# Kernel tuning notes

Measured on AMD Instinct MI355X. Metric: run time of the kernel, lower is better.

## Reference

```python
import jax, jax.numpy as jnp
import numpy as np

NEG_SLOPE = 0.2  # PyG GATConv default
EPS = 1e-16      # PyG softmax denominator epsilon

N_NODES = 100000
N_EDGES = 1600000
NFEAT = 768
NHID = 128
N_GRAPHS = 128


def setup_inputs() -> dict:
    key = jax.random.key(0)
    ks = jax.random.split(key, 12)
    x = jax.random.normal(ks[0], (N_NODES, NFEAT), dtype=jnp.float32)
    edge_index = jax.random.randint(ks[1], (2, N_EDGES), 0, N_NODES, dtype=jnp.int64)
    batch = jnp.sort(jax.random.randint(ks[2], (N_NODES,), 0, N_GRAPHS, dtype=jnp.int64))
    s = 1.0 / np.sqrt(NFEAT)
    sh = 1.0 / np.sqrt(NHID)
    params = {
        'W': jax.random.normal(ks[3], (NFEAT, NHID), dtype=jnp.float32) * s,
        'att_src': jax.random.normal(ks[4], (NHID,), dtype=jnp.float32) * sh,
        'att_dst': jax.random.normal(ks[5], (NHID,), dtype=jnp.float32) * sh,
        'b_conv': jnp.zeros((NHID,), dtype=jnp.float32),
        'W0': jax.random.normal(ks[6], (NFEAT, NHID), dtype=jnp.float32) * s,
        'b0': jnp.zeros((NHID,), dtype=jnp.float32),
        'W1': jax.random.normal(ks[7], (2 * NHID, NHID), dtype=jnp.float32) * sh,
        'b1': jnp.zeros((NHID,), dtype=jnp.float32),
        'W2': jax.random.normal(ks[8], (NHID, 2), dtype=jnp.float32) * sh,
        'b2': jnp.zeros((2,), dtype=jnp.float32),
    }
    return dict(x=x, edge_index=edge_index, batch=batch, num_graphs=N_GRAPHS, **params)


def _gat_conv(x, edge_index, W, att_src, att_dst, b_conv):
    N = x.shape[0]
    h = x @ W                               # [N, nhid]
    # add self loops (PyG default)
    loop = jnp.arange(N, dtype=edge_index.dtype)
    src = jnp.concatenate([edge_index[0], loop])
    dst = jnp.concatenate([edge_index[1], loop])
    a_src = h @ att_src                     # [N]
    a_dst = h @ att_dst                     # [N]
    e = a_src[src] + a_dst[dst]             # [E+N]
    e = jnp.where(e > 0, e, NEG_SLOPE * e)  # leaky relu
    # segment softmax over edges grouped by destination node
    m = jax.ops.segment_max(e, dst, num_segments=N)
    expe = jnp.exp(e - m[dst])
    denom = jax.ops.segment_sum(expe, dst, num_segments=N)
    alpha = expe / (denom[dst] + EPS)       # [E+N]
    out = jax.ops.segment_sum(alpha[:, None] * h[src], dst, num_segments=N)
    return out + b_conv


def reference(x, edge_index, batch, num_graphs, W, att_src, att_dst, b_conv,
              W0, b0, W1, b1, W2, b2):
    h = jax.nn.relu(_gat_conv(x, edge_index, W, att_src, att_dst, b_conv))  # [N, nhid]
    # global max pool per graph
    x1 = jax.ops.segment_max(h, batch, num_segments=num_graphs)             # [G, nhid]
    # root node of each graph = first node with batch == idx (batch sorted)
    roots = jnp.searchsorted(batch, jnp.arange(num_graphs, dtype=batch.dtype))
    news = jax.nn.relu(x[roots] @ W0 + b0)                                  # [G, nhid]
    z = jnp.concatenate([x1, news], axis=1)                                 # [G, 2*nhid]
    z = jax.nn.relu(z @ W1 + b1)
    logp = jax.nn.log_softmax(z @ W2 + b2, axis=1)                          # [G, 2]
    return (logp, x1, logp)
```

## Files before the change

kernel.cpp:

```cpp
#include <hip/hip_runtime.h>
#include <hip/hip_bf16.h>

#define NFEAT 768
#define NHID 128
#define NEG_SLOPE 0.2f
#define SM_EPS 1e-16f
#define CAP 96

#define BROWS 32
#define QSTRIDE 200

#define BSH 7
#define BNODES 128
#define CAPB 3072

#define SMEM_BYTES 26624

typedef __attribute__((ext_vector_type(8))) short bf16x8s;
typedef __attribute__((ext_vector_type(4))) float f32x4;

__device__ inline float bf2f(unsigned short u) {
    return __uint_as_float(((unsigned int)u) << 16);
}
__device__ inline unsigned short f2bf(float f) {
    union { __hip_bfloat16 b; unsigned short u; } c;
    c.b = __float2bfloat16(f);
    return c.u;
}
__device__ inline ushort4 cvt4(float4 v) {
    union { ushort4 u4; __hip_bfloat162 h[2]; } u;
    u.h[0] = __float22bfloat162_rn(float2{v.x, v.y});
    u.h[1] = __float22bfloat162_rn(float2{v.z, v.w});
    return u.u4;
}

__global__ void prep_wt(const float* __restrict__ W, unsigned short* __restrict__ Wt) {
    int idx = blockIdx.x * 256 + threadIdx.x;
    if (idx >= NFEAT * NHID) return;
    int k = idx >> 7, n = idx & 127;
    Wt[(size_t)n * NFEAT + k] = f2bf(W[idx]);
}

__global__ __launch_bounds__(256) void gemm_scatter_k(
        const float* __restrict__ x, const unsigned short* __restrict__ Wt,
        const float* __restrict__ att_src, const float* __restrict__ att_dst,
        unsigned short* __restrict__ hbf, float* __restrict__ a_src,
        float* __restrict__ a_dst, int M, int GB,
        const int* __restrict__ esrc, const int* __restrict__ edst,
        int* __restrict__ bktCnt, int* __restrict__ ebkt, int E, int nbkt) {
    __shared__ __align__(16) unsigned char smem[SMEM_BYTES];
    const int tid = threadIdx.x;

    if (blockIdx.x < GB) {
        unsigned short* At = (unsigned short*)smem;
        float* asum = (float*)(smem + 25600);
        const int lane = tid & 63;
        const int wid = tid >> 6;
        const int r0 = blockIdx.x * BROWS;
        if (r0 >= M) return;

        int qrow[6], qcol[6];
#pragma unroll
        for (int i = 0; i < 6; ++i) {
            int idx = i * 256 + tid;
            qrow[i] = idx / 48;
            qcol[i] = (idx % 48) * 4;
        }
        float4 xbuf[6];
        auto qload = [&](int q) {
#pragma unroll
            for (int i = 0; i < 6; ++i) {
                int gr = r0 + qrow[i]; if (gr >= M) gr = M - 1;
                xbuf[i] = *(const float4*)(x + (size_t)gr * NFEAT + q * 192 + qcol[i]);
            }
        };
        auto qwrite = [&](int q) {
#pragma unroll
            for (int i = 0; i < 6; ++i)
                *(ushort4*)(&At[(q & 1) * (BROWS * QSTRIDE) + qrow[i] * QSTRIDE + qcol[i]]) = cvt4(xbuf[i]);
        };

        const int rl = lane & 15;
        const int kc = (lane >> 4) * 8;
        const int c0 = wid * 32;
        const unsigned short* bp0 = Wt + (size_t)(c0 + rl) * NFEAT + kc;
        const unsigned short* bp1 = bp0 + (size_t)16 * NFEAT;

        qload(0); qwrite(0);
        __syncthreads();

        f32x4 acc[2][2] = {};
#pragma unroll
        for (int q = 0; q < 4; ++q) {
            bf16x8s bq0[6], bq1[6];
#pragma unroll
            for (int l = 0; l < 6; ++l) {
                int ks = q * 6 + l;
                bq0[l] = *(const bf16x8s*)(bp0 + ks * 32);
                bq1[l] = *(const bf16x8s*)(bp1 + ks * 32);
            }
            if (q < 3) qload(q + 1);
            const unsigned short* A0 = &At[(q & 1) * (BROWS * QSTRIDE) + rl * QSTRIDE + kc];
            const unsigned short* A1 = A0 + 16 * QSTRIDE;
#pragma unroll
            for (int l = 0; l < 6; ++l) {
                bf16x8s a0 = *(const bf16x8s*)(A0 + l * 32);
                bf16x8s a1 = *(const bf16x8s*)(A1 + l * 32);
                acc[0][0] = __builtin_amdgcn_mfma_f32_16x16x32_bf16(a0, bq0[l], acc[0][0], 0, 0, 0);
                acc[0][1] = __builtin_amdgcn_mfma_f32_16x16x32_bf16(a0, bq1[l], acc[0][1], 0, 0, 0);
                acc[1][0] = __builtin_amdgcn_mfma_f32_16x16x32_bf16(a1, bq0[l], acc[1][0], 0, 0, 0);
                acc[1][1] = __builtin_amdgcn_mfma_f32_16x16x32_bf16(a1, bq1[l], acc[1][1], 0, 0, 0);
            }
            if (q < 3) { qwrite(q + 1); __syncthreads(); }
        }

        const int cc = lane & 15;
        const int cg = lane >> 4;
        float as_[2], ad_[2];
#pragma unroll
        for (int n = 0; n < 2; ++n) {
            as_[n] = att_src[c0 + n * 16 + cc];
            ad_[n] = att_dst[c0 + n * 16 + cc];
        }
#pragma unroll
        for (int mfr = 0; mfr < 2; ++mfr) {
#pragma unroll
            for (int j = 0; j < 4; ++j) {
                int row = mfr * 16 + cg * 4 + j;
                int gr = r0 + row;
                float ps = 0.f, pd = 0.f;
#pragma unroll
                for (int n = 0; n < 2; ++n) {
                    float v = acc[mfr][n][j];
                    if (gr < M) hbf[(size_t)gr * NHID + c0 + n * 16 + cc] = f2bf(v);
                    ps += v * as_[n]; pd += v * ad_[n];
                }
#pragma unroll
                for (int d = 1; d < 16; d <<= 1) { ps += __shfl_xor(ps, d); pd += __shfl_xor(pd, d); }
                if (cc == 0) { asum[(0 * 4 + wid) * BROWS + row] = ps; asum[(1 * 4 + wid) * BROWS + row] = pd; }
            }
        }
        __syncthreads();
        if (tid < 64) {
            int row = tid & 31, sd = tid >> 5;
            float v = asum[(sd * 4 + 0) * BROWS + row] + asum[(sd * 4 + 1) * BROWS + row]
                    + asum[(sd * 4 + 2) * BROWS + row] + asum[(sd * 4 + 3) * BROWS + row];
            int gr = r0 + row;
            if (gr < M) { if (sd) a_dst[gr] = v; else a_src[gr] = v; }
        }
    } else {
        int* hist = (int*)smem;
        int* base = hist + 1024;
        int* curs = base + 1024;
        const int bid = blockIdx.x - GB;
        const int e0 = bid * 2048 + tid * 8;
        for (int b = tid; b < nbkt; b += 256) hist[b] = 0;
        __syncthreads();

        int dv[8], sv[8];
        int nval = 0;
        if (e0 + 7 < E) {
            int4 d0 = *(const int4*)(edst + e0), d1 = *(const int4*)(edst + e0 + 4);
            int4 s0 = *(const int4*)(esrc + e0), s1 = *(const int4*)(esrc + e0 + 4);
            dv[0] = d0.x; dv[1] = d0.y; dv[2] = d0.z; dv[3] = d0.w;
            dv[4] = d1.x; dv[5] = d1.y; dv[6] = d1.z; dv[7] = d1.w;
            sv[0] = s0.x; sv[1] = s0.y; sv[2] = s0.z; sv[3] = s0.w;
            sv[4] = s1.x; sv[5] = s1.y; sv[6] = s1.z; sv[7] = s1.w;
            nval = 8;
        } else {
            for (int i = 0; i < 8; ++i) {
                int e = e0 + i;
                if (e < E) { dv[nval] = edst[e]; sv[nval] = esrc[e]; ++nval; }
            }
        }
        for (int i = 0; i < nval; ++i) atomicAdd(&hist[dv[i] >> BSH], 1);
        __syncthreads();
        for (int b = tid; b < nbkt; b += 256) {
            int h = hist[b];
            if (h) base[b] = atomicAdd(bktCnt + b, h);
            curs[b] = 0;
        }
        __syncthreads();
        for (int i = 0; i < nval; ++i) {
            int b = dv[i] >> BSH;
            int pos = base[b] + atomicAdd(&curs[b], 1);
            if (pos < CAPB)
                ebkt[(size_t)b * CAPB + pos] = ((dv[i] & (BNODES - 1)) << 18) | sv[i];
        }
    }
}

__global__ __launch_bounds__(128) void csrb_k(const int* __restrict__ bktCnt,
                                              const int* __restrict__ ebkt,
                                              int* __restrict__ deg, int* __restrict__ off,
                                              int* __restrict__ csr, int N) {
    __shared__ int hist[BNODES], scn[BNODES], curs[BNODES];
    const int b = blockIdx.x, t = threadIdx.x;
    const int cnt = min(bktCnt[b], CAPB);
    const int* eb = ebkt + (size_t)b * CAPB;
    const int csrb = b * (CAPB + BNODES);
    const int node = (b << BSH) + t;

    hist[t] = 0;
    __syncthreads();
    for (int i = t; i < cnt; i += BNODES) atomicAdd(&hist[eb[i] >> 18], 1);
    __syncthreads();
    int tot = hist[t] + (node < N ? 1 : 0);
    scn[t] = tot;
    __syncthreads();
    for (int d = 1; d < BNODES; d <<= 1) {
        int x = (t >= d) ? scn[t - d] : 0;
        __syncthreads();
        scn[t] += x;
        __syncthreads();
    }
    int excl = scn[t] - tot;
    if (node < N) { deg[node] = tot; off[node] = csrb + excl; }
    curs[t] = excl;
    __syncthreads();
    for (int i = t; i < cnt; i += BNODES) {
        int v = eb[i];
        int pos = atomicAdd(&curs[v >> 18], 1);
        csr[csrb + pos] = v & 0x3FFFF;
    }
    __syncthreads();
    if (node < N) csr[csrb + curs[t]] = node;
}

__global__ __launch_bounds__(256) void aggregate_k(const int* __restrict__ off,
                                                   const int* __restrict__ deg,
                                                   const int* __restrict__ csr,
                                                   const float* __restrict__ a_src,
                                                   const float* __restrict__ a_dst,
                                                   const unsigned short* __restrict__ hbf,
                                                   const float* __restrict__ b_conv,
                                                   unsigned short* __restrict__ hrelu, int N) {
    __shared__ int   ssh[4][CAP];
    __shared__ float wsh[4][CAP];
    int wid = threadIdx.x >> 6, lane = threadIdx.x & 63;
    int dst = blockIdx.x * 4 + wid;
    if (dst >= N) return;
    int start = off[dst], cnt = deg[dst];
    float ad = a_dst[dst];

    float m = -1e30f;
    for (int j = lane; j < cnt; j += 64) {
        int s = csr[start + j];
        float e = a_src[s] + ad;
        e = e > 0.f ? e : NEG_SLOPE * e;
        if (j < CAP) { ssh[wid][j] = s; wsh[wid][j] = e; }
        m = fmaxf(m, e);
    }
#pragma unroll
    for (int d = 32; d; d >>= 1) m = fmaxf(m, __shfl_xor(m, d));

    float denom = 0.f;
    for (int j = lane; j < cnt; j += 64) {
        float e;
        if (j < CAP) e = wsh[wid][j];
        else {
            int s = csr[start + j];
            e = a_src[s] + ad;
            e = e > 0.f ? e : NEG_SLOPE * e;
        }
        float w = __expf(e - m);
        if (j < CAP) wsh[wid][j] = w;
        denom += w;
    }
#pragma unroll
    for (int d = 32; d; d >>= 1) denom += __shfl_xor(denom, d);

    const int el = lane >> 4;
    const int fg = lane & 15;
    float acc[8] = {};
    const unsigned short* hp8 = hbf + fg * 8;

    auto fma8 = [&](int s, float w) {
        bf16x8s hv = *(const bf16x8s*)(hp8 + (size_t)s * NHID);
#pragma unroll
        for (int i = 0; i < 8; ++i)
            acc[i] += w * bf2f((unsigned short)hv[i]);
    };

    if (cnt <= CAP) {
        int quads = cnt >> 2;
#pragma unroll 2
        for (int p = 0; p < quads; ++p) {
            int jj = p * 4 + el;
            fma8(ssh[wid][jj], wsh[wid][jj]);
        }
        int rem = cnt & 3;
        if (rem) {
            int jb = cnt & ~3;
            int jj = jb + (el < rem ? el : 0);
            float w = (el < rem) ? wsh[wid][jj] : 0.f;
            fma8(ssh[wid][jj], w);
        }
    } else {
        for (int j = 0; j < cnt; j += 4) {
            int jj = j + el;
            int s; float w;
            if (jj < cnt) {
                if (jj < CAP) { s = ssh[wid][jj]; w = wsh[wid][jj]; }
                else {
                    s = csr[start + jj];
                    float e = a_src[s] + ad;
                    e = e > 0.f ? e : NEG_SLOPE * e;
                    w = __expf(e - m);
                }
            } else { s = ssh[wid][0]; w = 0.f; }
            fma8(s, w);
        }
    }
#pragma unroll
    for (int i = 0; i < 8; ++i) {
        acc[i] += __shfl_xor(acc[i], 16);
        acc[i] += __shfl_xor(acc[i], 32);
    }

    if (lane < 16) {
        float inv = 1.f / (denom + SM_EPS);
        union { bf16x8s v; unsigned short u[8]; } ob;
#pragma unroll
        for (int i = 0; i < 8; ++i)
            ob.u[i] = f2bf(fmaxf(acc[i] * inv + b_conv[fg * 8 + i], 0.f));
        *(bf16x8s*)(&hrelu[(size_t)dst * NHID + fg * 8]) = ob.v;
    }
}

__global__ __launch_bounds__(256) void pool_max(const unsigned short* __restrict__ hrelu,
                                                const int* __restrict__ batch,
                                                float* __restrict__ x1, int N) {
    int wid = threadIdx.x >> 6, lane = threadIdx.x & 63;
    int n0 = blockIdx.x * 256 + wid * 64;
    if (n0 >= N) return;
    int gcur = batch[n0];
    float v0 = 0.f, v1 = 0.f;
    int end = min(n0 + 64, N);
    for (int n = n0; n < end; ++n) {
        int g = batch[n];
        if (g != gcur) {
            atomicMax((int*)&x1[gcur * NHID + lane * 2],     __float_as_int(v0));
            atomicMax((int*)&x1[gcur * NHID + lane * 2 + 1], __float_as_int(v1));
            v0 = v1 = 0.f; gcur = g;
        }
        ushort2 hv = *(const ushort2*)(hrelu + (size_t)n * NHID + lane * 2);
        v0 = fmaxf(v0, bf2f(hv.x)); v1 = fmaxf(v1, bf2f(hv.y));
    }
    atomicMax((int*)&x1[gcur * NHID + lane * 2],     __float_as_int(v0));
    atomicMax((int*)&x1[gcur * NHID + lane * 2 + 1], __float_as_int(v1));
}

__global__ __launch_bounds__(128) void tail_k(const float* __restrict__ x,
                                              const int* __restrict__ batch,
                                              const float* __restrict__ W0,
                                              const float* __restrict__ b0,
                                              const float* __restrict__ W1,
                                              const float* __restrict__ b1,
                                              const float* __restrict__ W2,
                                              const float* __restrict__ b2,
                                              const float* __restrict__ x1,
                                              float* __restrict__ logp0,
                                              float* __restrict__ logp1, int N) {
    __shared__ float xr[NFEAT];
    __shared__ float zin[2 * NHID];
    __shared__ float z[NHID];
    __shared__ float lg[2];
    int g = blockIdx.x, t = threadIdx.x;
    int lo = 0, hi = N;
    while (lo < hi) { int mid = (lo + hi) >> 1; if (batch[mid] < g) lo = mid + 1; else hi = mid; }
    int root = min(lo, N - 1);
    const float* xp = x + (size_t)root * NFEAT;
    for (int i = t; i < NFEAT; i += 128) xr[i] = xp[i];
    zin[t] = x1[(size_t)g * NHID + t];
    __syncthreads();
    float acc = b0[t];
#pragma unroll 8
    for (int k = 0; k < NFEAT; ++k) acc += xr[k] * W0[(size_t)k * NHID + t];
    zin[NHID + t] = fmaxf(acc, 0.f);
    __syncthreads();
    float a1 = b1[t];
#pragma unroll 8
    for (int k = 0; k < 2 * NHID; ++k) a1 += zin[k] * W1[(size_t)k * NHID + t];
    z[t] = fmaxf(a1, 0.f);
    __syncthreads();
    if (t < 2) {
        float a = b2[t];
        for (int k = 0; k < NHID; ++k) a += z[k] * W2[k * 2 + t];
        lg[t] = a;
    }
    __syncthreads();
    if (t == 0) {
        float mx = fmaxf(lg[0], lg[1]);
        float lse = mx + logf(expf(lg[0] - mx) + expf(lg[1] - mx));
        float p0 = lg[0] - lse, p1 = lg[1] - lse;
        logp0[g * 2] = p0; logp0[g * 2 + 1] = p1;
        logp1[g * 2] = p0; logp1[g * 2 + 1] = p1;
    }
}

extern "C" void kernel_launch(void* const* d_in, const int* in_sizes, int n_in,
                              void* d_out, int out_size, void* d_ws, size_t ws_size,
                              hipStream_t stream) {
    const float* x        = (const float*)d_in[0];
    const int*   eidx     = (const int*)d_in[1];
    const int*   batch    = (const int*)d_in[2];
    const float* W        = (const float*)d_in[4];
    const float* att_src  = (const float*)d_in[5];
    const float* att_dst  = (const float*)d_in[6];
    const float* b_conv   = (const float*)d_in[7];
    const float* W0       = (const float*)d_in[8];
    const float* b0       = (const float*)d_in[9];
    const float* W1       = (const float*)d_in[10];
    const float* b1       = (const float*)d_in[11];
    const float* W2       = (const float*)d_in[12];
    const float* b2       = (const float*)d_in[13];

    const int N = in_sizes[2];
    const int E = in_sizes[1] / 2;
    const int G = out_size / (2 + NHID + 2);
    const int nbkt = (N + BNODES - 1) / BNODES;

    char* ws = (char*)d_ws;
    size_t o = 0;
    auto alloc = [&](size_t bytes) -> char* {
        char* p = ws + o; o += (bytes + 255) & ~(size_t)255; return p;
    };
    unsigned short* hbf   = (unsigned short*)alloc((size_t)N * NHID * 2);
    unsigned short* hrelu = (unsigned short*)alloc((size_t)N * NHID * 2);
    float* a_src          = (float*)alloc((size_t)N * 4);
    float* a_dst          = (float*)alloc((size_t)N * 4);
    unsigned short* Wt    = (unsigned short*)alloc((size_t)NHID * NFEAT * 2);
    int* deg              = (int*)alloc((size_t)N * 4);
    int* off              = (int*)alloc((size_t)N * 4);
    int* bktCnt           = (int*)alloc((size_t)nbkt * 4);
    int* ebkt             = (int*)alloc((size_t)nbkt * CAPB * 4);
    int* csr              = (int*)alloc((size_t)nbkt * (CAPB + BNODES) * 4);

    float* out_logp  = (float*)d_out;
    float* out_x1    = out_logp + 2 * G;
    float* out_logp2 = out_x1 + (size_t)G * NHID;

    hipMemsetAsync(d_out, 0, (size_t)out_size * 4, stream);
    hipMemsetAsync(bktCnt, 0, (size_t)nbkt * 4, stream);

    prep_wt<<<(NFEAT * NHID + 255) / 256, 256, 0, stream>>>(W, Wt);
    const int GB = (N + BROWS - 1) / BROWS;
    const int SB = (E + 2047) / 2048;
    gemm_scatter_k<<<GB + SB, 256, 0, stream>>>(x, Wt, att_src, att_dst,
                                                hbf, a_src, a_dst, N, GB,
                                                eidx, eidx + E, bktCnt, ebkt, E, nbkt);
    csrb_k<<<nbkt, 128, 0, stream>>>(bktCnt, ebkt, deg, off, csr, N);
    aggregate_k<<<(N + 3) / 4, 256, 0, stream>>>(off, deg, csr, a_src, a_dst, hbf, b_conv,
                                                 hrelu, N);
    pool_max<<<(N + 255) / 256, 256, 0, stream>>>(hrelu, batch, out_x1, N);
    tail_k<<<G, 128, 0, stream>>>(x, batch, W0, b0, W1, b1, W2, b2, out_x1,
                                  out_logp, out_logp2, N);
}
```

Before: 316.7 us.

## Fuse CSR build, attention aggregation and max-pool into one bucket kernel

Merges the bucket CSR construction, the per-destination softmax aggregation and the global max-pool into a single kernel with one block per 128-node bucket. The CSR lives in shared memory and the ReLU outputs are reduced straight into the per-graph max with atomics. This removes the global csr/deg/off/hrelu buffers, their round trips through memory, and two launches. In exchange there are only about 782 blocks of 256 threads, each wave walking 32 destinations serially, so latency hiding and occupancy may drop compared with one wave per destination.

```diff
diff --git a/kernel.cpp b/kernel.cpp
--- a/kernel.cpp
+++ b/kernel.cpp
@@ -190,165 +190,142 @@
     }
 }
 
-__global__ __launch_bounds__(128) void csrb_k(const int* __restrict__ bktCnt,
-                                              const int* __restrict__ ebkt,
-                                              int* __restrict__ deg, int* __restrict__ off,
-                                              int* __restrict__ csr, int N) {
+__global__ __launch_bounds__(256) void bucket_agg_k(
+        const int* __restrict__ bktCnt, const int* __restrict__ ebkt,
+        const float* __restrict__ a_src, const float* __restrict__ a_dst,
+        const unsigned short* __restrict__ hbf, const float* __restrict__ b_conv,
+        const int* __restrict__ batch, float* __restrict__ x1out, int N) {
+    __shared__ int csr_l[CAPB + BNODES];
     __shared__ int hist[BNODES], scn[BNODES], curs[BNODES];
-    const int b = blockIdx.x, t = threadIdx.x;
+    __shared__ float wsh[4][CAP];
+    const int b = blockIdx.x, tid = threadIdx.x;
+    const int wid = tid >> 6, lane = tid & 63;
     const int cnt = min(bktCnt[b], CAPB);
     const int* eb = ebkt + (size_t)b * CAPB;
-    const int csrb = b * (CAPB + BNODES);
-    const int node = (b << BSH) + t;
-
-    hist[t] = 0;
-    __syncthreads();
-    for (int i = t; i < cnt; i += BNODES) atomicAdd(&hist[eb[i] >> 18], 1);
-    __syncthreads();
-    int tot = hist[t] + (node < N ? 1 : 0);
-    scn[t] = tot;
+
+    if (tid < BNODES) hist[tid] = 0;
+    __syncthreads();
+    for (int i = tid; i < cnt; i += 256) atomicAdd(&hist[eb[i] >> 18], 1);
+    __syncthreads();
+    int tot = 0;
+    if (tid < BNODES) {
+        int node = (b << BSH) + tid;
+        tot = hist[tid] + (node < N ? 1 : 0);
+        scn[tid] = tot;
+    }
     __syncthreads();
     for (int d = 1; d < BNODES; d <<= 1) {
-        int x = (t >= d) ? scn[t - d] : 0;
-        __syncthreads();
-        scn[t] += x;
-        __syncthreads();
-    }
-    int excl = scn[t] - tot;
-    if (node < N) { deg[node] = tot; off[node] = csrb + excl; }
-    curs[t] = excl;
-    __syncthreads();
-    for (int i = t; i < cnt; i += BNODES) {
+        int xv = 0;
+        if (tid < BNODES && tid >= d) xv = scn[tid - d];
+        __syncthreads();
+        if (tid < BNODES) scn[tid] += xv;
+        __syncthreads();
+    }
+    if (tid < BNODES) curs[tid] = scn[tid] - tot;
+    __syncthreads();
+    for (int i = tid; i < cnt; i += 256) {
         int v = eb[i];
         int pos = atomicAdd(&curs[v >> 18], 1);
-        csr[csrb + pos] = v & 0x3FFFF;
-    }
-    __syncthreads();
-    if (node < N) csr[csrb + curs[t]] = node;
-}
-
-__global__ __launch_bounds__(256) void aggregate_k(const int* __restrict__ off,
-                                                   const int* __restrict__ deg,
-                                                   const int* __restrict__ csr,
-                                                   const float* __restrict__ a_src,
-                                                   const float* __restrict__ a_dst,
-                                                   const unsigned short* __restrict__ hbf,
-                                                   const float* __restrict__ b_conv,
-                                                   unsigned short* __restrict__ hrelu, int N) {
-    __shared__ int   ssh[4][CAP];
-    __shared__ float wsh[4][CAP];
-    int wid = threadIdx.x >> 6, lane = threadIdx.x & 63;
-    int dst = blockIdx.x * 4 + wid;
-    if (dst >= N) return;
-    int start = off[dst], cnt = deg[dst];
-    float ad = a_dst[dst];
-
-    float m = -1e30f;
-    for (int j = lane; j < cnt; j += 64) {
-        int s = csr[start + j];
-        float e = a_src[s] + ad;
-        e = e > 0.f ? e : NEG_SLOPE * e;
-        if (j < CAP) { ssh[wid][j] = s; wsh[wid][j] = e; }
-        m = fmaxf(m, e);
-    }
-#pragma unroll
-    for (int d = 32; d; d >>= 1) m = fmaxf(m, __shfl_xor(m, d));
-
-    float denom = 0.f;
-    for (int j = lane; j < cnt; j += 64) {
-        float e;
-        if (j < CAP) e = wsh[wid][j];
-        else {
-            int s = csr[start + j];
-            e = a_src[s] + ad;
+        csr_l[pos] = v & 0x3FFFF;
+    }
+    __syncthreads();
+    if (tid < BNODES) {
+        int node = (b << BSH) + tid;
+        if (node < N) csr_l[curs[tid]] = node;
+    }
+    __syncthreads();
+
+    const int fg = lane & 15;
+    float bcv[8];
+#pragma unroll
+    for (int i = 0; i < 8; ++i) bcv[i] = b_conv[fg * 8 + i];
+    const unsigned short* hp8 = hbf + fg * 8;
+
+    float pmax[8] = {};
+    int gcur = -1;
+    auto flush = [&]() {
+        if (gcur >= 0 && lane < 16) {
+            float* row = x1out + (size_t)gcur * NHID + fg * 8;
+#pragma unroll
+            for (int i = 0; i < 8; ++i)
+                atomicMax((int*)(row + i), __float_as_int(pmax[i]));
+        }
+    };
+
+    const int ld0 = wid * 32;
+    for (int ld = ld0; ld < ld0 + 32; ++ld) {
+        int node = (b << BSH) + ld;
+        if (node >= N) break;
+        int end = scn[ld];
+        int start = ld ? scn[ld - 1] : 0;
+        int cnt_d = end - start;
+        float ad = a_dst[node];
+
+        float m = -1e30f;
+        for (int j = lane; j < cnt_d; j += 64) {
+            int s = csr_l[start + j];
+            float e = a_src[s] + ad;
             e = e > 0.f ? e : NEG_SLOPE * e;
-        }
-        float w = __expf(e - m);
-        if (j < CAP) wsh[wid][j] = w;
-        denom += w;
-    }
-#pragma unroll
-    for (int d = 32; d; d >>= 1) denom += __shfl_xor(denom, d);
-
-    const int el = lane >> 4;
-    const int fg = lane & 15;
-    float acc[8] = {};
-    const unsigned short* hp8 = hbf + fg * 8;
-
-    auto fma8 = [&](int s, float w) {
-        bf16x8s hv = *(const bf16x8s*)(hp8 + (size_t)s * NHID);
-#pragma unroll
-        for (int i = 0; i < 8; ++i)
-            acc[i] += w * bf2f((unsigned short)hv[i]);
-    };
-
-    if (cnt <= CAP) {
-        int quads = cnt >> 2;
-#pragma unroll 2
-        for (int p = 0; p < quads; ++p) {
-            int jj = p * 4 + el;
-            fma8(ssh[wid][jj], wsh[wid][jj]);
-        }
-        int rem = cnt & 3;
-        if (rem) {
-            int jb = cnt & ~3;
-            int jj = jb + (el < rem ? el : 0);
-            float w = (el < rem) ? wsh[wid][jj] : 0.f;
-            fma8(ssh[wid][jj], w);
-        }
-    } else {
-        for (int j = 0; j < cnt; j += 4) {
+            if (j < CAP) wsh[wid][j] = e;
+            m = fmaxf(m, e);
+        }
+#pragma unroll
+        for (int d = 32; d; d >>= 1) m = fmaxf(m, __shfl_xor(m, d));
+
+        float denom = 0.f;
+        for (int j = lane; j < cnt_d; j += 64) {
+            float e;
+            if (j < CAP) e = wsh[wid][j];
+            else {
+                int s = csr_l[start + j];
+                e = a_src[s] + ad;
+                e = e > 0.f ? e : NEG_SLOPE * e;
+            }
+            float w = __expf(e - m);
+            if (j < CAP) wsh[wid][j] = w;
+            denom += w;
+        }
+#pragma unroll
+        for (int d = 32; d; d >>= 1) denom += __shfl_xor(denom, d);
+
+        const int el = lane >> 4;
+        float acc[8] = {};
+        for (int j = 0; j < cnt_d; j += 4) {
             int jj = j + el;
             int s; float w;
-            if (jj < cnt) {
-                if (jj < CAP) { s = ssh[wid][jj]; w = wsh[wid][jj]; }
+            if (jj < cnt_d) {
+                s = csr_l[start + jj];
+                if (jj < CAP) w = wsh[wid][jj];
                 else {
-                    s = csr[start + jj];
                     float e = a_src[s] + ad;
                     e = e > 0.f ? e : NEG_SLOPE * e;
                     w = __expf(e - m);
                 }
-            } else { s = ssh[wid][0]; w = 0.f; }
-            fma8(s, w);
-        }
-    }
-#pragma unroll
-    for (int i = 0; i < 8; ++i) {
-        acc[i] += __shfl_xor(acc[i], 16);
-        acc[i] += __shfl_xor(acc[i], 32);
-    }
-
-    if (lane < 16) {
+            } else { s = csr_l[start]; w = 0.f; }
+            bf16x8s hv = *(const bf16x8s*)(hp8 + (size_t)s * NHID);
+#pragma unroll
+            for (int i = 0; i < 8; ++i)
+                acc[i] += w * bf2f((unsigned short)hv[i]);
+        }
+#pragma unroll
+        for (int i = 0; i < 8; ++i) {
+            acc[i] += __shfl_xor(acc[i], 16);
+            acc[i] += __shfl_xor(acc[i], 32);
+        }
+
         float inv = 1.f / (denom + SM_EPS);
-        union { bf16x8s v; unsigned short u[8]; } ob;
+        int g = batch[node];
+        if (g != gcur) {
+            flush();
+            gcur = g;
+#pragma unroll
+            for (int i = 0; i < 8; ++i) pmax[i] = 0.f;
+        }
 #pragma unroll
         for (int i = 0; i < 8; ++i)
-            ob.u[i] = f2bf(fmaxf(acc[i] * inv + b_conv[fg * 8 + i], 0.f));
-        *(bf16x8s*)(&hrelu[(size_t)dst * NHID + fg * 8]) = ob.v;
-    }
-}
-
-__global__ __launch_bounds__(256) void pool_max(const unsigned short* __restrict__ hrelu,
-                                                const int* __restrict__ batch,
-                                                float* __restrict__ x1, int N) {
-    int wid = threadIdx.x >> 6, lane = threadIdx.x & 63;
-    int n0 = blockIdx.x * 256 + wid * 64;
-    if (n0 >= N) return;
-    int gcur = batch[n0];
-    float v0 = 0.f, v1 = 0.f;
-    int end = min(n0 + 64, N);
-    for (int n = n0; n < end; ++n) {
-        int g = batch[n];
-        if (g != gcur) {
-            atomicMax((int*)&x1[gcur * NHID + lane * 2],     __float_as_int(v0));
-            atomicMax((int*)&x1[gcur * NHID + lane * 2 + 1], __float_as_int(v1));
-            v0 = v1 = 0.f; gcur = g;
-        }
-        ushort2 hv = *(const ushort2*)(hrelu + (size_t)n * NHID + lane * 2);
-        v0 = fmaxf(v0, bf2f(hv.x)); v1 = fmaxf(v1, bf2f(hv.y));
-    }
-    atomicMax((int*)&x1[gcur * NHID + lane * 2],     __float_as_int(v0));
-    atomicMax((int*)&x1[gcur * NHID + lane * 2 + 1], __float_as_int(v1));
+            pmax[i] = fmaxf(pmax[i], fmaxf(acc[i] * inv + bcv[i], 0.f));
+    }
+    flush();
 }
 
 __global__ __launch_bounds__(128) void tail_k(const float* __restrict__ x,
@@ -427,15 +404,11 @@
         char* p = ws + o; o += (bytes + 255) & ~(size_t)255; return p;
     };
     unsigned short* hbf   = (unsigned short*)alloc((size_t)N * NHID * 2);
-    unsigned short* hrelu = (unsigned short*)alloc((size_t)N * NHID * 2);
     float* a_src          = (float*)alloc((size_t)N * 4);
     float* a_dst          = (float*)alloc((size_t)N * 4);
     unsigned short* Wt    = (unsigned short*)alloc((size_t)NHID * NFEAT * 2);
-    int* deg              = (int*)alloc((size_t)N * 4);
-    int* off              = (int*)alloc((size_t)N * 4);
     int* bktCnt           = (int*)alloc((size_t)nbkt * 4);
     int* ebkt             = (int*)alloc((size_t)nbkt * CAPB * 4);
-    int* csr              = (int*)alloc((size_t)nbkt * (CAPB + BNODES) * 4);
 
     float* out_logp  = (float*)d_out;
     float* out_x1    = out_logp + 2 * G;
@@ -450,10 +423,8 @@
     gemm_scatter_k<<<GB + SB, 256, 0, stream>>>(x, Wt, att_src, att_dst,
                                                 hbf, a_src, a_dst, N, GB,
                                                 eidx, eidx + E, bktCnt, ebkt, E, nbkt);
-    csrb_k<<<nbkt, 128, 0, stream>>>(bktCnt, ebkt, deg, off, csr, N);
-    aggregate_k<<<(N + 3) / 4, 256, 0, stream>>>(off, deg, csr, a_src, a_dst, hbf, b_conv,
-                                                 hrelu, N);
-    pool_max<<<(N + 255) / 256, 256, 0, stream>>>(hrelu, batch, out_x1, N);
+    bucket_agg_k<<<nbkt, 256, 0, stream>>>(bktCnt, ebkt, a_src, a_dst, hbf, b_conv,
+                                           batch, out_x1, N);
     tail_k<<<G, 128, 0, stream>>>(x, batch, W0, b0, W1, b1, W2, b2, out_x1,
                                   out_logp, out_logp2, N);
 }
```

Measured after the change: 320.8 us. No clear change (+1.3%).

## Fuse CSR build into GEMM/scatter kernel with a global completion counter

Applied to the files above, without the earlier changes.

Removes the separate csrb_k launch by appending CSR-building blocks to the fused GEMM+scatter grid. These blocks spin on a global atomic counter until every scatter block has signalled completion, so CSR construction can overlap with the tail of the GEMM blocks and one kernel launch is saved. This relies on the scatter blocks being scheduled before the waiting CSR blocks (block-order assumption), and the spinning blocks occupy CU slots. CSR blocks now use 256 threads, with half of them idle during the scan phases.

```diff
diff --git a/kernel.cpp b/kernel.cpp
--- a/kernel.cpp
+++ b/kernel.cpp
@@ -45,9 +45,11 @@
         const float* __restrict__ x, const unsigned short* __restrict__ Wt,
         const float* __restrict__ att_src, const float* __restrict__ att_dst,
         unsigned short* __restrict__ hbf, float* __restrict__ a_src,
-        float* __restrict__ a_dst, int M, int GB,
+        float* __restrict__ a_dst, int M, int GB, int SB,
         const int* __restrict__ esrc, const int* __restrict__ edst,
-        int* __restrict__ bktCnt, int* __restrict__ ebkt, int E, int nbkt) {
+        int* __restrict__ bktCnt, int* __restrict__ ebkt, int E, int nbkt,
+        int* __restrict__ scDone,
+        int* __restrict__ deg, int* __restrict__ off, int* __restrict__ csr, int N) {
     __shared__ __align__(16) unsigned char smem[SMEM_BYTES];
     const int tid = threadIdx.x;
 
@@ -148,7 +150,7 @@
             int gr = r0 + row;
             if (gr < M) { if (sd) a_dst[gr] = v; else a_src[gr] = v; }
         }
-    } else {
+    } else if (blockIdx.x < GB + SB) {
         int* hist = (int*)smem;
         int* base = hist + 1024;
         int* curs = base + 1024;
@@ -187,44 +189,61 @@
             if (pos < CAPB)
                 ebkt[(size_t)b * CAPB + pos] = ((dv[i] & (BNODES - 1)) << 18) | sv[i];
         }
-    }
-}
-
-__global__ __launch_bounds__(128) void csrb_k(const int* __restrict__ bktCnt,
-                                              const int* __restrict__ ebkt,
-                                              int* __restrict__ deg, int* __restrict__ off,
-                                              int* __restrict__ csr, int N) {
-    __shared__ int hist[BNODES], scn[BNODES], curs[BNODES];
-    const int b = blockIdx.x, t = threadIdx.x;
-    const int cnt = min(bktCnt[b], CAPB);
-    const int* eb = ebkt + (size_t)b * CAPB;
-    const int csrb = b * (CAPB + BNODES);
-    const int node = (b << BSH) + t;
-
-    hist[t] = 0;
-    __syncthreads();
-    for (int i = t; i < cnt; i += BNODES) atomicAdd(&hist[eb[i] >> 18], 1);
-    __syncthreads();
-    int tot = hist[t] + (node < N ? 1 : 0);
-    scn[t] = tot;
-    __syncthreads();
-    for (int d = 1; d < BNODES; d <<= 1) {
-        int x = (t >= d) ? scn[t - d] : 0;
-        __syncthreads();
-        scn[t] += x;
-        __syncthreads();
-    }
-    int excl = scn[t] - tot;
-    if (node < N) { deg[node] = tot; off[node] = csrb + excl; }
-    curs[t] = excl;
-    __syncthreads();
-    for (int i = t; i < cnt; i += BNODES) {
-        int v = eb[i];
-        int pos = atomicAdd(&curs[v >> 18], 1);
-        csr[csrb + pos] = v & 0x3FFFF;
-    }
-    __syncthreads();
-    if (node < N) csr[csrb + curs[t]] = node;
+        __syncthreads();
+        if (tid == 0) {
+            __threadfence();
+            __hip_atomic_fetch_add(scDone, 1, __ATOMIC_RELEASE, __HIP_MEMORY_SCOPE_AGENT);
+        }
+    } else {
+        int* hist = (int*)smem;
+        int* scn  = hist + BNODES;
+        int* curs = scn + BNODES;
+        const int b = blockIdx.x - GB - SB;
+        if (tid == 0) {
+            while (__hip_atomic_load(scDone, __ATOMIC_ACQUIRE, __HIP_MEMORY_SCOPE_AGENT) < SB)
+                __builtin_amdgcn_s_sleep(64);
+        }
+        __syncthreads();
+        __threadfence();
+        const int cnt = min(bktCnt[b], CAPB);
+        const int* eb = ebkt + (size_t)b * CAPB;
+        const int csrb = b * (CAPB + BNODES);
+        if (tid < BNODES) hist[tid] = 0;
+        __syncthreads();
+        for (int i = tid; i < cnt; i += 256) atomicAdd(&hist[eb[i] >> 18], 1);
+        __syncthreads();
+        int tot = 0;
+        if (tid < BNODES) {
+            int node = (b << BSH) + tid;
+            tot = hist[tid] + (node < N ? 1 : 0);
+            scn[tid] = tot;
+        }
+        __syncthreads();
+        for (int d = 1; d < BNODES; d <<= 1) {
+            int xv = 0;
+            if (tid < BNODES && tid >= d) xv = scn[tid - d];
+            __syncthreads();
+            if (tid < BNODES) scn[tid] += xv;
+            __syncthreads();
+        }
+        if (tid < BNODES) {
+            int node = (b << BSH) + tid;
+            int excl = scn[tid] - tot;
+            if (node < N) { deg[node] = tot; off[node] = csrb + excl; }
+            curs[tid] = excl;
+        }
+        __syncthreads();
+        for (int i = tid; i < cnt; i += 256) {
+            int v = eb[i];
+            int pos = atomicAdd(&curs[v >> 18], 1);
+            csr[csrb + pos] = v & 0x3FFFF;
+        }
+        __syncthreads();
+        if (tid < BNODES) {
+            int node = (b << BSH) + tid;
+            if (node < N) csr[csrb + curs[tid]] = node;
+        }
+    }
 }
 
 __global__ __launch_bounds__(256) void aggregate_k(const int* __restrict__ off,
@@ -433,7 +452,8 @@
     unsigned short* Wt    = (unsigned short*)alloc((size_t)NHID * NFEAT * 2);
     int* deg              = (int*)alloc((size_t)N * 4);
     int* off              = (int*)alloc((size_t)N * 4);
-    int* bktCnt           = (int*)alloc((size_t)nbkt * 4);
+    int* bktCnt           = (int*)alloc((size_t)(nbkt + 1) * 4);
+    int* scDone           = bktCnt + nbkt;
     int* ebkt             = (int*)alloc((size_t)nbkt * CAPB * 4);
     int* csr              = (int*)alloc((size_t)nbkt * (CAPB + BNODES) * 4);
 
@@ -442,15 +462,16 @@
     float* out_logp2 = out_x1 + (size_t)G * NHID;
 
     hipMemsetAsync(d_out, 0, (size_t)out_size * 4, stream);
-    hipMemsetAsync(bktCnt, 0, (size_t)nbkt * 4, stream);
+    hipMemsetAsync(bktCnt, 0, (size_t)(nbkt + 1) * 4, stream);
 
     prep_wt<<<(NFEAT * NHID + 255) / 256, 256, 0, stream>>>(W, Wt);
     const int GB = (N + BROWS - 1) / BROWS;
     const int SB = (E + 2047) / 2048;
-    gemm_scatter_k<<<GB + SB, 256, 0, stream>>>(x, Wt, att_src, att_dst,
-                                                hbf, a_src, a_dst, N, GB,
-                                                eidx, eidx + E, bktCnt, ebkt, E, nbkt);
-    csrb_k<<<nbkt, 128, 0, stream>>>(bktCnt, ebkt, deg, off, csr, N);
+    const int CB = nbkt;
+    gemm_scatter_k<<<GB + SB + CB, 256, 0, stream>>>(x, Wt, att_src, att_dst,
+                                                     hbf, a_src, a_dst, N, GB, SB,
+                                                     eidx, eidx + E, bktCnt, ebkt, E, nbkt,
+                                                     scDone, deg, off, csr, N);
     aggregate_k<<<(N + 3) / 4, 256, 0, stream>>>(off, deg, csr, a_src, a_dst, hbf, b_conv,
                                                  hrelu, N);
     pool_max<<<(N + 255) / 256, 256, 0, stream>>>(hrelu, batch, out_x1, N);
```

Result: slower. 538.5 us (+70.1%).
